# Performance work log

Measured on AMD Instinct MI355X. Metric: run time of the kernel, lower is better.

## Reference

```python
import jax, jax.numpy as jnp
import numpy as np

B, T, D, H, L = 64, 512, 512, 512, 2


def setup_inputs() -> dict:
    key = jax.random.key(0)
    ks = jax.random.split(key, 9)
    std = 1.0 / np.sqrt(H)
    u = lambda k, shape: jax.random.uniform(k, shape, jnp.float32, -std, std)
    return {
        "x": jax.random.normal(ks[0], (B, T, D), jnp.float32),
        "Wx0": u(ks[1], (4 * H, D)), "bx0": u(ks[2], (4 * H,)),
        "Wh0": u(ks[3], (4 * H, H)), "bh0": u(ks[4], (4 * H,)),
        "Wx1": u(ks[5], (4 * H, H)), "bx1": u(ks[6], (4 * H,)),
        "Wh1": u(ks[7], (4 * H, H)), "bh1": u(ks[8], (4 * H,)),
    }


def _lstm_layer(x_seq, Wx, bx, Wh, bh):
    # x_seq: [T, B, D_in] -> hidden sequence [T, B, H]
    h0 = jnp.zeros((x_seq.shape[1], Wh.shape[1]), x_seq.dtype)
    c0 = jnp.zeros_like(h0)
    # precompute input projections for all steps (one big GEMM)
    xg = jnp.einsum('tbd,gd->tbg', x_seq, Wx) + bx + bh  # [T, B, 4H]

    def step(carry, xg_t):
        h, c = carry
        gates = xg_t + h @ Wh.T
        f, i, g, o = jnp.split(gates, 4, axis=1)
        f = jax.nn.sigmoid(f)
        i = jax.nn.sigmoid(i)
        g = jnp.tanh(g)
        o = jax.nn.sigmoid(o)
        c = f * c + i * g
        h = o * jnp.tanh(c)
        return (h, c), h

    (_, _), hs = jax.lax.scan(step, (h0, c0), xg)
    return hs


def reference(x, Wx0, bx0, Wh0, bh0, Wx1, bx1, Wh1, bh1):
    xs = jnp.transpose(x, (1, 0, 2))  # [T, B, D]
    h1 = _lstm_layer(xs, Wx0, bx0, Wh0, bh0)   # [T, B, H]
    h2 = _lstm_layer(h1, Wx1, bx1, Wh1, bh1)   # [T, B, H]
    return h2[-1]  # last hidden state of top layer: [B, H]
```

## Files before the change

kernel.cpp:

```cpp
#include <hip/hip_runtime.h>
#include <hip/hip_bf16.h>
#include <stdint.h>

#define T_STEPS 512
#define BATCH   64
#define HID     512
#define DIN     512
#define G4      2048
#define HBLK_T  32768
#define RING    16
#define SENT8   0xFFFFFFFFFFFFFFFFull

typedef __attribute__((ext_vector_type(8))) short bf16x8;
typedef __attribute__((ext_vector_type(4))) float f32x4;
typedef __attribute__((ext_vector_type(4))) unsigned short us4;
typedef unsigned long long ull;

static __device__ __forceinline__ unsigned short f2bf(float f) {
  union { float f; unsigned u; } v; v.f = f;
  unsigned r = v.u + 0x7FFFu + ((v.u >> 16) & 1u);
  return (unsigned short)(r >> 16);
}
static __device__ __forceinline__ float bf2f(unsigned short s) {
  union { unsigned u; float f; } v; v.u = ((unsigned)s) << 16;
  return v.f;
}
static __device__ __forceinline__ float sigf(float x) { return 1.f / (1.f + __expf(-x)); }
static __device__ __forceinline__ float tanh_fast(float x) {
  x = fminf(15.f, fmaxf(-15.f, x));
  float e = __expf(2.f * x);
  return (e - 1.f) / (e + 1.f);
}

__global__ __launch_bounds__(256) void xb_cvt(const float* __restrict__ x,
                                              unsigned short* __restrict__ xb) {
  const long c  = (long)blockIdx.x * blockDim.x + threadIdx.x;
  const int b   = (int)(c >> 15);
  const int rem = (int)(c & 32767);
  const int t   = rem >> 6;
  const int k8  = rem & 63;
  const float* src = x + ((long)b * T_STEPS + t) * DIN + k8 * 8;
  f32x4 v0 = *(const f32x4*)src;
  f32x4 v1 = *(const f32x4*)(src + 4);
  union { unsigned short s[8]; bf16x8 v; } u;
  #pragma unroll
  for (int e = 0; e < 4; ++e) { u.s[e] = f2bf(v0[e]); u.s[4 + e] = f2bf(v1[e]); }
  *(bf16x8*)(xb + ((long)t * BATCH + b) * DIN + k8 * 8) = u.v;
}

__global__ __launch_bounds__(192, 1) void fused_rec(
    const float* __restrict__ Wh0, const float* __restrict__ Wx0,
    const float* __restrict__ Wh1, const float* __restrict__ Wx1,
    const float* __restrict__ bx0, const float* __restrict__ bh0,
    const float* __restrict__ bx1, const float* __restrict__ bh1,
    const unsigned short* __restrict__ xb,
    unsigned short* __restrict__ hseq1,
    unsigned short* __restrict__ hseq2,
    float* __restrict__ out,
    int T) {
  __shared__ unsigned short wx0l[32 * 512];
  __shared__ unsigned short whl0[32 * 512];
  __shared__ unsigned short whl1[32 * 1024];
  __shared__ __align__(16) unsigned short ring[RING][512];
  __shared__ __align__(16) unsigned short hsc[2][128];
  __shared__ int p_done, l0_done;

  const int bid  = blockIdx.x;
  const int gq   = bid & 3;
  const int j    = bid >> 2;
  const int wv   = threadIdx.x >> 6;
  const int lane = threadIdx.x & 63;
  const int hidbase = j * 8;
  const int n16  = lane & 15;
  const int q    = lane >> 4;
  const int kof  = q * 8;
  const int bloc = q * 4;
  const int rr0 = n16, rr1 = 16 + n16;
  const int grow0 = (rr0 >> 3) * HID + hidbase + (rr0 & 7);
  const int grow1 = (rr1 >> 3) * HID + hidbase + (rr1 & 7);
  const int rdbase = gq * 128 + n16 * 8;
  const int myblk  = (j * 4 + gq) * 128;

  if (threadIdx.x == 0) { p_done = 0; l0_done = 0; }

  auto cv8 = [](const float* s) -> bf16x8 {
    f32x4 a = *(const f32x4*)s, b = *(const f32x4*)(s + 4);
    union { unsigned short u[8]; bf16x8 v; } w;
    #pragma unroll
    for (int e = 0; e < 4; ++e) { w.u[e] = f2bf(a[e]); w.u[4 + e] = f2bf(b[e]); }
    return w.v;
  };
  if (wv == 0) {
    for (int r = 0; r < 32; ++r) {
      const long grow = (long)(r >> 3) * HID + hidbase + (r & 7);
      bf16x8 v = cv8(Wh0 + grow * HID + lane * 8);
      *(bf16x8*)((char*)whl0 + r * 1024 + ((lane * 16) ^ ((r & 7) << 4))) = v;
    }
  } else if (wv == 1) {
    for (int r = 0; r < 32; ++r) {
      const long grow = (long)(r >> 3) * HID + hidbase + (r & 7);
      bf16x8 va = cv8(Wx1 + grow * HID + lane * 8);
      bf16x8 vb = cv8(Wh1 + grow * HID + lane * 8);
      const int rb = r * 2048;
      *(bf16x8*)((char*)whl1 + rb + ((lane * 16) ^ ((r & 7) << 4))) = va;
      *(bf16x8*)((char*)whl1 + rb + ((1024 + lane * 16) ^ ((r & 7) << 4))) = vb;
    }
  } else {
    for (int r = 0; r < 32; ++r) {
      const long grow = (long)(r >> 3) * HID + hidbase + (r & 7);
      bf16x8 v = cv8(Wx0 + grow * HID + lane * 8);
      *(bf16x8*)((char*)wx0l + r * 1024 + ((lane * 16) ^ ((r & 7) << 4))) = v;
    }
  }
  __syncthreads();

  if (wv == 0) {
    float c4[4] = {0.f, 0.f, 0.f, 0.f};
    for (int t = 0; t < T; ++t) {
      ull lo[16], hi[16];
      const ull* hp = (const ull*)(hseq1 + (long)(t - 1) * HBLK_T + rdbase);
      if (t > 0) {
        #pragma unroll
        for (int kk = 0; kk < 16; ++kk) {
          const int boff = (kk * 4 + q) * 128;
          lo[kk] = __hip_atomic_load(hp + boff,     __ATOMIC_RELAXED, __HIP_MEMORY_SCOPE_AGENT);
          hi[kk] = __hip_atomic_load(hp + boff + 1, __ATOMIC_RELAXED, __HIP_MEMORY_SCOPE_AGENT);
        }
      }
      while (__hip_atomic_load(&p_done, __ATOMIC_ACQUIRE, __HIP_MEMORY_SCOPE_WORKGROUP) < t + 1) {}
      const int s = t & (RING - 1);
      us4 xv0 = *(const us4*)&ring[s][n16 * 16 + q * 4];
      us4 xv1 = *(const us4*)&ring[s][(16 + n16) * 16 + q * 4];
      if (lane == 0)
        __hip_atomic_store(&l0_done, t + 1, __ATOMIC_RELEASE, __HIP_MEMORY_SCOPE_WORKGROUP);

      f32x4 acc0 = {0.f,0.f,0.f,0.f}, acc1 = {0.f,0.f,0.f,0.f};
      if (t > 0) {
        for (;;) {
          int bad = 0;
          #pragma unroll
          for (int kk = 0; kk < 16; ++kk) bad |= (lo[kk] == SENT8) | (hi[kk] == SENT8);
          if (!__any(bad)) break;
          #pragma unroll
          for (int kk = 0; kk < 16; ++kk) {
            const int boff = (kk * 4 + q) * 128;
            lo[kk] = __hip_atomic_load(hp + boff,     __ATOMIC_RELAXED, __HIP_MEMORY_SCOPE_AGENT);
            hi[kk] = __hip_atomic_load(hp + boff + 1, __ATOMIC_RELAXED, __HIP_MEMORY_SCOPE_AGENT);
          }
        }
        #pragma unroll
        for (int kk = 0; kk < 16; ++kk) {
          union { ull qq[2]; bf16x8 v; } u; u.qq[0] = lo[kk]; u.qq[1] = hi[kk];
          const int colb = (kof + kk * 32) * 2;
          bf16x8 b0 = *(const bf16x8*)((const char*)whl0 + rr0 * 1024 + (colb ^ ((rr0 & 7) << 4)));
          bf16x8 b1 = *(const bf16x8*)((const char*)whl0 + rr1 * 1024 + (colb ^ ((rr1 & 7) << 4)));
          acc0 = __builtin_amdgcn_mfma_f32_16x16x32_bf16(u.v, b0, acc0, 0, 0, 0);
          acc1 = __builtin_amdgcn_mfma_f32_16x16x32_bf16(u.v, b1, acc1, 0, 0, 0);
        }
      }
      #pragma unroll
      for (int r = 0; r < 4; ++r) { acc0[r] += bf2f(xv0[r]); acc1[r] += bf2f(xv1[r]); }

      f32x4 o0, o1;
      #pragma unroll
      for (int r = 0; r < 4; ++r) {
        o0[r] = __shfl_xor(acc0[r], 8, 64);
        o1[r] = __shfl_xor(acc1[r], 8, 64);
      }
      if (n16 < 8) {
        #pragma unroll
        for (int r = 0; r < 4; ++r) {
          const float fg = sigf(acc0[r]);
          const float ig = sigf(o0[r]);
          const float gg = tanh_fast(acc1[r]);
          const float og = sigf(o1[r]);
          const float cn = fg * c4[r] + ig * gg;
          c4[r] = cn;
          const float h = og * tanh_fast(cn);
          *(unsigned short*)((char*)hsc[0] + (bloc + r) * 16 + n16 * 2) = f2bf(h);
        }
      }
      asm volatile("s_waitcnt lgkmcnt(0)" ::: "memory");
      if (lane < 32) {
        ull v8 = *(const ull*)((const char*)hsc[0] + lane * 8);
        ull* dst = (ull*)(hseq1 + (long)t * HBLK_T + myblk) + lane;
        __hip_atomic_store(dst, v8, __ATOMIC_RELAXED, __HIP_MEMORY_SCOPE_AGENT);
      }
    }
  } else if (wv == 1) {
    float c4[4] = {0.f, 0.f, 0.f, 0.f};
    const float b0v = bx1[grow0] + bh1[grow0];
    const float b1v = bx1[grow1] + bh1[grow1];
    for (int t = 0; t < T; ++t) {
      ull la[16], ha[16], lb[16], hb[16];
      const ull* pa = (const ull*)(hseq1 + (long)t * HBLK_T + rdbase);
      const ull* pb = (const ull*)(hseq2 + (long)(t - 1) * HBLK_T + rdbase);
      #pragma unroll
      for (int kk = 0; kk < 16; ++kk) {
        const int boff = (kk * 4 + q) * 128;
        la[kk] = __hip_atomic_load(pa + boff,     __ATOMIC_RELAXED, __HIP_MEMORY_SCOPE_AGENT);
        ha[kk] = __hip_atomic_load(pa + boff + 1, __ATOMIC_RELAXED, __HIP_MEMORY_SCOPE_AGENT);
      }
      if (t > 0) {
        #pragma unroll
        for (int kk = 0; kk < 16; ++kk) {
          const int boff = (kk * 4 + q) * 128;
          lb[kk] = __hip_atomic_load(pb + boff,     __ATOMIC_RELAXED, __HIP_MEMORY_SCOPE_AGENT);
          hb[kk] = __hip_atomic_load(pb + boff + 1, __ATOMIC_RELAXED, __HIP_MEMORY_SCOPE_AGENT);
        }
      }
      for (;;) {
        int bad = 0;
        #pragma unroll
        for (int kk = 0; kk < 16; ++kk) bad |= (la[kk] == SENT8) | (ha[kk] == SENT8);
        if (!__any(bad)) break;
        #pragma unroll
        for (int kk = 0; kk < 16; ++kk) {
          const int boff = (kk * 4 + q) * 128;
          la[kk] = __hip_atomic_load(pa + boff,     __ATOMIC_RELAXED, __HIP_MEMORY_SCOPE_AGENT);
          ha[kk] = __hip_atomic_load(pa + boff + 1, __ATOMIC_RELAXED, __HIP_MEMORY_SCOPE_AGENT);
        }
      }
      f32x4 acc0 = {0.f,0.f,0.f,0.f}, acc1 = {0.f,0.f,0.f,0.f};
      #pragma unroll
      for (int kk = 0; kk < 16; ++kk) {
        union { ull qq[2]; bf16x8 v; } u; u.qq[0] = la[kk]; u.qq[1] = ha[kk];
        const int colb = (kof + kk * 32) * 2;
        bf16x8 b0 = *(const bf16x8*)((const char*)whl1 + rr0 * 2048 + (colb ^ ((rr0 & 7) << 4)));
        bf16x8 b1 = *(const bf16x8*)((const char*)whl1 + rr1 * 2048 + (colb ^ ((rr1 & 7) << 4)));
        acc0 = __builtin_amdgcn_mfma_f32_16x16x32_bf16(u.v, b0, acc0, 0, 0, 0);
        acc1 = __builtin_amdgcn_mfma_f32_16x16x32_bf16(u.v, b1, acc1, 0, 0, 0);
      }
      if (t > 0) {
        for (;;) {
          int bad = 0;
          #pragma unroll
          for (int kk = 0; kk < 16; ++kk) bad |= (lb[kk] == SENT8) | (hb[kk] == SENT8);
          if (!__any(bad)) break;
          #pragma unroll
          for (int kk = 0; kk < 16; ++kk) {
            const int boff = (kk * 4 + q) * 128;
            lb[kk] = __hip_atomic_load(pb + boff,     __ATOMIC_RELAXED, __HIP_MEMORY_SCOPE_AGENT);
            hb[kk] = __hip_atomic_load(pb + boff + 1, __ATOMIC_RELAXED, __HIP_MEMORY_SCOPE_AGENT);
          }
        }
        #pragma unroll
        for (int kk = 0; kk < 16; ++kk) {
          union { ull qq[2]; bf16x8 v; } u; u.qq[0] = lb[kk]; u.qq[1] = hb[kk];
          const int colb = 1024 + (kof + kk * 32) * 2;
          bf16x8 b0 = *(const bf16x8*)((const char*)whl1 + rr0 * 2048 + (colb ^ ((rr0 & 7) << 4)));
          bf16x8 b1 = *(const bf16x8*)((const char*)whl1 + rr1 * 2048 + (colb ^ ((rr1 & 7) << 4)));
          acc0 = __builtin_amdgcn_mfma_f32_16x16x32_bf16(u.v, b0, acc0, 0, 0, 0);
          acc1 = __builtin_amdgcn_mfma_f32_16x16x32_bf16(u.v, b1, acc1, 0, 0, 0);
        }
      }
      #pragma unroll
      for (int r = 0; r < 4; ++r) { acc0[r] += b0v; acc1[r] += b1v; }

      f32x4 o0, o1;
      #pragma unroll
      for (int r = 0; r < 4; ++r) {
        o0[r] = __shfl_xor(acc0[r], 8, 64);
        o1[r] = __shfl_xor(acc1[r], 8, 64);
      }
      if (n16 < 8) {
        const int hid = hidbase + n16;
        #pragma unroll
        for (int r = 0; r < 4; ++r) {
          const float fg = sigf(acc0[r]);
          const float ig = sigf(o0[r]);
          const float gg = tanh_fast(acc1[r]);
          const float og = sigf(o1[r]);
          const float cn = fg * c4[r] + ig * gg;
          c4[r] = cn;
          const float h = og * tanh_fast(cn);
          *(unsigned short*)((char*)hsc[1] + (bloc + r) * 16 + n16 * 2) = f2bf(h);
          if (t == T - 1) out[(long)(gq * 16 + bloc + r) * HID + hid] = h;
        }
      }
      asm volatile("s_waitcnt lgkmcnt(0)" ::: "memory");
      if (lane < 32) {
        ull v8 = *(const ull*)((const char*)hsc[1] + lane * 8);
        ull* dst = (ull*)(hseq2 + (long)t * HBLK_T + myblk) + lane;
        __hip_atomic_store(dst, v8, __ATOMIC_RELAXED, __HIP_MEMORY_SCOPE_AGENT);
      }
    }
  } else {
    const float bsP0 = bx0[grow0] + bh0[grow0];
    const float bsP1 = bx0[grow1] + bh0[grow1];
    for (int t = 0; t < T; ++t) {
      while (t - __hip_atomic_load(&l0_done, __ATOMIC_RELAXED, __HIP_MEMORY_SCOPE_WORKGROUP) >= RING)
        __builtin_amdgcn_s_sleep(1);
      const unsigned short* xp = xb + ((long)t * BATCH + gq * 16 + n16) * DIN + kof;
      f32x4 a0 = {0.f,0.f,0.f,0.f}, a1 = {0.f,0.f,0.f,0.f};
      #pragma unroll
      for (int kk = 0; kk < 16; ++kk) {
        bf16x8 av = *(const bf16x8*)(xp + kk * 32);
        const int colb = (kof + kk * 32) * 2;
        bf16x8 b0 = *(const bf16x8*)((const char*)wx0l + rr0 * 1024 + (colb ^ ((rr0 & 7) << 4)));
        bf16x8 b1 = *(const bf16x8*)((const char*)wx0l + rr1 * 1024 + (colb ^ ((rr1 & 7) << 4)));
        a0 = __builtin_amdgcn_mfma_f32_16x16x32_bf16(av, b0, a0, 0, 0, 0);
        a1 = __builtin_amdgcn_mfma_f32_16x16x32_bf16(av, b1, a1, 0, 0, 0);
      }
      us4 w0, w1;
      #pragma unroll
      for (int r = 0; r < 4; ++r) {
        w0[r] = f2bf(a0[r] + bsP0);
        w1[r] = f2bf(a1[r] + bsP1);
      }
      const int s = t & (RING - 1);
      *(us4*)&ring[s][n16 * 16 + q * 4] = w0;
      *(us4*)&ring[s][(16 + n16) * 16 + q * 4] = w1;
      if (lane == 0)
        __hip_atomic_store(&p_done, t + 1, __ATOMIC_RELEASE, __HIP_MEMORY_SCOPE_WORKGROUP);
    }
  }
}

extern "C" void kernel_launch(void* const* d_in, const int* in_sizes, int n_in,
                              void* d_out, int out_size, void* d_ws, size_t ws_size,
                              hipStream_t stream) {
  const float* x   = (const float*)d_in[0];
  const float* Wx0 = (const float*)d_in[1];
  const float* bx0 = (const float*)d_in[2];
  const float* Wh0 = (const float*)d_in[3];
  const float* bh0 = (const float*)d_in[4];
  const float* Wx1 = (const float*)d_in[5];
  const float* bx1 = (const float*)d_in[6];
  const float* Wh1 = (const float*)d_in[7];
  const float* bh1 = (const float*)d_in[8];

  char* ws = (char*)d_ws;
  size_t off = 0;
  auto alloc = [&](size_t bytes) -> char* {
    char* p = ws + off; off += (bytes + 255) & ~(size_t)255; return p;
  };
  unsigned short* xb    = (unsigned short*)alloc((size_t)T_STEPS * BATCH * DIN * 2);
  unsigned short* hseq1 = (unsigned short*)alloc((size_t)T_STEPS * HBLK_T * 2);
  unsigned short* hseq2 = (unsigned short*)alloc((size_t)T_STEPS * HBLK_T * 2);

  hipMemsetAsync(hseq1, 0xFF, (size_t)T_STEPS * HBLK_T * 2, stream);
  hipMemsetAsync(hseq2, 0xFF, (size_t)T_STEPS * HBLK_T * 2, stream);

  xb_cvt<<<8192, 256, 0, stream>>>(x, xb);

  fused_rec<<<256, 192, 0, stream>>>(Wh0, Wx0, Wh1, Wx1,
                                     bx0, bh0, bx1, bh1,
                                     xb, hseq1, hseq2, (float*)d_out, T_STEPS);
}
```

Measured before the change: 2.278 ms.

## Precompute layer-0 input projection in a separate GEMM kernel instead of in-loop producer wave

Removes the producer wavefront that computed the layer-0 input projection per timestep inside the persistent recurrent kernel and passed it through a shared-memory ring. A new proj_kernel computes all timesteps' gate inputs up front (with bias) into a global bf16 buffer, and the recurrent kernel now reads them directly from global memory. This shrinks the recurrent block to two waves and removes the ring handshakes. In exchange it adds a separate GEMM launch and a 128 MB intermediate buffer that must be written and read back, and it reorders the hseq polling loop.

Result: slower. 2.504 ms (+10.0%).

```diff
diff --git a/kernel.cpp b/kernel.cpp
--- a/kernel.cpp
+++ b/kernel.cpp
@@ -8,7 +8,6 @@
 #define DIN     512
 #define G4      2048
 #define HBLK_T  32768
-#define RING    16
 #define SENT8   0xFFFFFFFFFFFFFFFFull
 
 typedef __attribute__((ext_vector_type(8))) short bf16x8;
@@ -32,38 +31,87 @@
   return (e - 1.f) / (e + 1.f);
 }
 
-__global__ __launch_bounds__(256) void xb_cvt(const float* __restrict__ x,
-                                              unsigned short* __restrict__ xb) {
-  const long c  = (long)blockIdx.x * blockDim.x + threadIdx.x;
-  const int b   = (int)(c >> 15);
-  const int rem = (int)(c & 32767);
-  const int t   = rem >> 6;
-  const int k8  = rem & 63;
-  const float* src = x + ((long)b * T_STEPS + t) * DIN + k8 * 8;
-  f32x4 v0 = *(const f32x4*)src;
-  f32x4 v1 = *(const f32x4*)(src + 4);
-  union { unsigned short s[8]; bf16x8 v; } u;
-  #pragma unroll
-  for (int e = 0; e < 4; ++e) { u.s[e] = f2bf(v0[e]); u.s[4 + e] = f2bf(v1[e]); }
-  *(bf16x8*)(xb + ((long)t * BATCH + b) * DIN + k8 * 8) = u.v;
-}
-
-__global__ __launch_bounds__(192, 1) void fused_rec(
-    const float* __restrict__ Wh0, const float* __restrict__ Wx0,
-    const float* __restrict__ Wh1, const float* __restrict__ Wx1,
-    const float* __restrict__ bx0, const float* __restrict__ bh0,
+__global__ void cvt_f32_bf16(const float* __restrict__ src, unsigned short* __restrict__ dst, long n) {
+  long i = (long)blockIdx.x * blockDim.x + threadIdx.x;
+  long st = (long)gridDim.x * blockDim.x;
+  for (; i < n; i += st) dst[i] = f2bf(src[i]);
+}
+
+__global__ __launch_bounds__(256) void proj_kernel(
+    const float* __restrict__ x,
+    const unsigned short* __restrict__ Wb,
+    const float* __restrict__ ba,
+    const float* __restrict__ bb,
+    unsigned short* __restrict__ xg) {
+  __shared__ unsigned short xt[64 * 512];
+  const int t   = blockIdx.x;
+  const int tid = threadIdx.x;
+
+  for (int i = 0; i < 16; ++i) {
+    const int c    = i * 256 + tid;
+    const int b    = c >> 6;
+    const int col8 = c & 63;
+    const float* src = x + ((long)b * T_STEPS + t) * DIN + col8 * 8;
+    f32x4 v0 = *(const f32x4*)(src);
+    f32x4 v1 = *(const f32x4*)(src + 4);
+    union { unsigned short s[8]; bf16x8 v; } u;
+    #pragma unroll
+    for (int e = 0; e < 4; ++e) { u.s[e] = f2bf(v0[e]); u.s[4 + e] = f2bf(v1[e]); }
+    const int byteoff = b * 1024 + ((col8 * 16) ^ ((b & 7) << 4));
+    *(bf16x8*)((char*)xt + byteoff) = u.v;
+  }
+  __syncthreads();
+
+  const int wv   = tid >> 6;
+  const int lane = tid & 63;
+  const int n16  = lane & 15;
+  const int q    = lane >> 4;
+  const int kof  = q * 8;
+
+  for (int gt = 0; gt < 32; ++gt) {
+    const int g0 = wv * 512 + gt * 16;
+    const unsigned short* ap = Wb + (long)(g0 + n16) * DIN + kof;
+    f32x4 acc[4];
+    #pragma unroll
+    for (int nb = 0; nb < 4; ++nb) acc[nb] = (f32x4){0.f, 0.f, 0.f, 0.f};
+    #pragma unroll
+    for (int kk = 0; kk < 16; ++kk) {
+      bf16x8 a = *(const bf16x8*)(ap + kk * 32);
+      const int colb = (kof + kk * 32) * 2;
+      #pragma unroll
+      for (int nb = 0; nb < 4; ++nb) {
+        const int row = nb * 16 + n16;
+        bf16x8 bv = *(const bf16x8*)((const char*)xt + row * 1024 + (colb ^ ((row & 7) << 4)));
+        acc[nb] = __builtin_amdgcn_mfma_f32_16x16x32_bf16(a, bv, acc[nb], 0, 0, 0);
+      }
+    }
+    const int m0 = q * 4;
+    #pragma unroll
+    for (int r = 0; r < 4; ++r) {
+      const int g = g0 + m0 + r;
+      const float bv = ba[g] + bb[g];
+      long base = ((long)t * G4 + g) * BATCH + n16;
+      xg[base +  0] = f2bf(acc[0][r] + bv);
+      xg[base + 16] = f2bf(acc[1][r] + bv);
+      xg[base + 32] = f2bf(acc[2][r] + bv);
+      xg[base + 48] = f2bf(acc[3][r] + bv);
+    }
+  }
+}
+
+__global__ __launch_bounds__(128, 1) void fused_rec(
+    const float* __restrict__ Wh0,
+    const float* __restrict__ Wx1,
+    const float* __restrict__ Wh1,
     const float* __restrict__ bx1, const float* __restrict__ bh1,
-    const unsigned short* __restrict__ xb,
+    const unsigned short* __restrict__ xg0,
     unsigned short* __restrict__ hseq1,
     unsigned short* __restrict__ hseq2,
     float* __restrict__ out,
     int T) {
-  __shared__ unsigned short wx0l[32 * 512];
   __shared__ unsigned short whl0[32 * 512];
   __shared__ unsigned short whl1[32 * 1024];
-  __shared__ __align__(16) unsigned short ring[RING][512];
   __shared__ __align__(16) unsigned short hsc[2][128];
-  __shared__ int p_done, l0_done;
 
   const int bid  = blockIdx.x;
   const int gq   = bid & 3;
@@ -81,8 +129,6 @@
   const int rdbase = gq * 128 + n16 * 8;
   const int myblk  = (j * 4 + gq) * 128;
 
-  if (threadIdx.x == 0) { p_done = 0; l0_done = 0; }
-
   auto cv8 = [](const float* s) -> bf16x8 {
     f32x4 a = *(const f32x4*)s, b = *(const f32x4*)(s + 4);
     union { unsigned short u[8]; bf16x8 v; } w;
@@ -96,7 +142,7 @@
       bf16x8 v = cv8(Wh0 + grow * HID + lane * 8);
       *(bf16x8*)((char*)whl0 + r * 1024 + ((lane * 16) ^ ((r & 7) << 4))) = v;
     }
-  } else if (wv == 1) {
+  } else {
     for (int r = 0; r < 32; ++r) {
       const long grow = (long)(r >> 3) * HID + hidbase + (r & 7);
       bf16x8 va = cv8(Wx1 + grow * HID + lane * 8);
@@ -105,49 +151,32 @@
       *(bf16x8*)((char*)whl1 + rb + ((lane * 16) ^ ((r & 7) << 4))) = va;
       *(bf16x8*)((char*)whl1 + rb + ((1024 + lane * 16) ^ ((r & 7) << 4))) = vb;
     }
-  } else {
-    for (int r = 0; r < 32; ++r) {
-      const long grow = (long)(r >> 3) * HID + hidbase + (r & 7);
-      bf16x8 v = cv8(Wx0 + grow * HID + lane * 8);
-      *(bf16x8*)((char*)wx0l + r * 1024 + ((lane * 16) ^ ((r & 7) << 4))) = v;
-    }
   }
   __syncthreads();
 
   if (wv == 0) {
     float c4[4] = {0.f, 0.f, 0.f, 0.f};
     for (int t = 0; t < T; ++t) {
-      ull lo[16], hi[16];
-      const ull* hp = (const ull*)(hseq1 + (long)(t - 1) * HBLK_T + rdbase);
-      if (t > 0) {
-        #pragma unroll
-        for (int kk = 0; kk < 16; ++kk) {
-          const int boff = (kk * 4 + q) * 128;
-          lo[kk] = __hip_atomic_load(hp + boff,     __ATOMIC_RELAXED, __HIP_MEMORY_SCOPE_AGENT);
-          hi[kk] = __hip_atomic_load(hp + boff + 1, __ATOMIC_RELAXED, __HIP_MEMORY_SCOPE_AGENT);
-        }
-      }
-      while (__hip_atomic_load(&p_done, __ATOMIC_ACQUIRE, __HIP_MEMORY_SCOPE_WORKGROUP) < t + 1) {}
-      const int s = t & (RING - 1);
-      us4 xv0 = *(const us4*)&ring[s][n16 * 16 + q * 4];
-      us4 xv1 = *(const us4*)&ring[s][(16 + n16) * 16 + q * 4];
-      if (lane == 0)
-        __hip_atomic_store(&l0_done, t + 1, __ATOMIC_RELEASE, __HIP_MEMORY_SCOPE_WORKGROUP);
+      us4 xv0 = *(const us4*)(xg0 + ((long)t * G4 + grow0) * BATCH + gq * 16 + bloc);
+      us4 xv1 = *(const us4*)(xg0 + ((long)t * G4 + grow1) * BATCH + gq * 16 + bloc);
 
       f32x4 acc0 = {0.f,0.f,0.f,0.f}, acc1 = {0.f,0.f,0.f,0.f};
       if (t > 0) {
-        for (;;) {
-          int bad = 0;
-          #pragma unroll
-          for (int kk = 0; kk < 16; ++kk) bad |= (lo[kk] == SENT8) | (hi[kk] == SENT8);
-          if (!__any(bad)) break;
+        const ull* hp = (const ull*)(hseq1 + (long)(t - 1) * HBLK_T + rdbase);
+        ull lo[16], hi[16];
+        int bad;
+        do {
+          bad = 0;
           #pragma unroll
           for (int kk = 0; kk < 16; ++kk) {
             const int boff = (kk * 4 + q) * 128;
             lo[kk] = __hip_atomic_load(hp + boff,     __ATOMIC_RELAXED, __HIP_MEMORY_SCOPE_AGENT);
             hi[kk] = __hip_atomic_load(hp + boff + 1, __ATOMIC_RELAXED, __HIP_MEMORY_SCOPE_AGENT);
           }
-        }
+          #pragma unroll
+          for (int kk = 0; kk < 16; ++kk)
+            bad |= (lo[kk] == SENT8) | (hi[kk] == SENT8);
+        } while (__any(bad));
         #pragma unroll
         for (int kk = 0; kk < 16; ++kk) {
           union { ull qq[2]; bf16x8 v; } u; u.qq[0] = lo[kk]; u.qq[1] = hi[kk];
@@ -187,7 +216,7 @@
         __hip_atomic_store(dst, v8, __ATOMIC_RELAXED, __HIP_MEMORY_SCOPE_AGENT);
       }
     }
-  } else if (wv == 1) {
+  } else {
     float c4[4] = {0.f, 0.f, 0.f, 0.f};
     const float b0v = bx1[grow0] + bh1[grow0];
     const float b1v = bx1[grow1] + bh1[grow1];
@@ -285,35 +314,6 @@
         __hip_atomic_store(dst, v8, __ATOMIC_RELAXED, __HIP_MEMORY_SCOPE_AGENT);
       }
     }
-  } else {
-    const float bsP0 = bx0[grow0] + bh0[grow0];
-    const float bsP1 = bx0[grow1] + bh0[grow1];
-    for (int t = 0; t < T; ++t) {
-      while (t - __hip_atomic_load(&l0_done, __ATOMIC_RELAXED, __HIP_MEMORY_SCOPE_WORKGROUP) >= RING)
-        __builtin_amdgcn_s_sleep(1);
-      const unsigned short* xp = xb + ((long)t * BATCH + gq * 16 + n16) * DIN + kof;
-      f32x4 a0 = {0.f,0.f,0.f,0.f}, a1 = {0.f,0.f,0.f,0.f};
-      #pragma unroll
-      for (int kk = 0; kk < 16; ++kk) {
-        bf16x8 av = *(const bf16x8*)(xp + kk * 32);
-        const int colb = (kof + kk * 32) * 2;
-        bf16x8 b0 = *(const bf16x8*)((const char*)wx0l + rr0 * 1024 + (colb ^ ((rr0 & 7) << 4)));
-        bf16x8 b1 = *(const bf16x8*)((const char*)wx0l + rr1 * 1024 + (colb ^ ((rr1 & 7) << 4)));
-        a0 = __builtin_amdgcn_mfma_f32_16x16x32_bf16(av, b0, a0, 0, 0, 0);
-        a1 = __builtin_amdgcn_mfma_f32_16x16x32_bf16(av, b1, a1, 0, 0, 0);
-      }
-      us4 w0, w1;
-      #pragma unroll
-      for (int r = 0; r < 4; ++r) {
-        w0[r] = f2bf(a0[r] + bsP0);
-        w1[r] = f2bf(a1[r] + bsP1);
-      }
-      const int s = t & (RING - 1);
-      *(us4*)&ring[s][n16 * 16 + q * 4] = w0;
-      *(us4*)&ring[s][(16 + n16) * 16 + q * 4] = w1;
-      if (lane == 0)
-        __hip_atomic_store(&p_done, t + 1, __ATOMIC_RELEASE, __HIP_MEMORY_SCOPE_WORKGROUP);
-    }
   }
 }
 
@@ -335,16 +335,17 @@
   auto alloc = [&](size_t bytes) -> char* {
     char* p = ws + off; off += (bytes + 255) & ~(size_t)255; return p;
   };
-  unsigned short* xb    = (unsigned short*)alloc((size_t)T_STEPS * BATCH * DIN * 2);
+  unsigned short* xg    = (unsigned short*)alloc((size_t)T_STEPS * G4 * BATCH * 2);
   unsigned short* hseq1 = (unsigned short*)alloc((size_t)T_STEPS * HBLK_T * 2);
   unsigned short* hseq2 = (unsigned short*)alloc((size_t)T_STEPS * HBLK_T * 2);
+  unsigned short* Wx0b  = (unsigned short*)alloc((size_t)G4 * DIN * 2);
 
   hipMemsetAsync(hseq1, 0xFF, (size_t)T_STEPS * HBLK_T * 2, stream);
   hipMemsetAsync(hseq2, 0xFF, (size_t)T_STEPS * HBLK_T * 2, stream);
 
-  xb_cvt<<<8192, 256, 0, stream>>>(x, xb);
-
-  fused_rec<<<256, 192, 0, stream>>>(Wh0, Wx0, Wh1, Wx1,
-                                     bx0, bh0, bx1, bh1,
-                                     xb, hseq1, hseq2, (float*)d_out, T_STEPS);
-}
+  cvt_f32_bf16<<<1024, 256, 0, stream>>>(Wx0, Wx0b, (long)G4 * DIN);
+
+  proj_kernel<<<T_STEPS, 256, 0, stream>>>(x, Wx0b, bx0, bh0, xg);
+  fused_rec<<<256, 128, 0, stream>>>(Wh0, Wx1, Wh1, bx1, bh1,
+                                     xg, hseq1, hseq2, (float*)d_out, T_STEPS);
+}
```
